# Kernel tuning notes

Hardware: AMD Instinct MI355X
Metric: run time of the kernel (lower is better)

Reference implementation:

```python
import jax, jax.numpy as jnp
import numpy as np

N_NODES = 100000


def gcn_layer(x, W, b, src, dst, n):
    # PyG GCNConv: add self-loops, symmetric degree normalization,
    # message = norm * (x @ W)[src], aggregated (sum) at dst, plus bias.
    loops = jnp.arange(n, dtype=src.dtype)
    s = jnp.concatenate([src, loops])  # [E+N]
    d = jnp.concatenate([dst, loops])  # [E+N]
    deg = jnp.zeros((n,), x.dtype).at[d].add(jnp.ones((s.shape[0],), x.dtype))
    dinv = jnp.where(deg > 0, jax.lax.rsqrt(deg), 0.0)
    norm = dinv[s] * dinv[d]  # [E+N]
    h = x @ W  # [N, out]
    msg = h[s] * norm[:, None]  # [E+N, out]
    out = jax.ops.segment_sum(msg, d, num_segments=n)
    return out + b


def setup_inputs() -> dict:
    key = jax.random.key(0)
    k1, k2, k3, k4 = jax.random.split(key, 4)
    in_dim, hid_dim, out_dim = 128, 128, 64
    x = jax.random.normal(k1, (N_NODES, in_dim), dtype=jnp.float32)
    edge_index = jax.random.randint(k2, (2, 1600000), 0, N_NODES, dtype=jnp.int64)
    W1 = jax.random.normal(k3, (in_dim, hid_dim), dtype=jnp.float32) / np.sqrt(in_dim)
    b1 = jnp.zeros((hid_dim,), jnp.float32)
    W2 = jax.random.normal(k4, (hid_dim, out_dim), dtype=jnp.float32) / np.sqrt(hid_dim)
    b2 = jnp.zeros((out_dim,), jnp.float32)
    return {"x": x, "edge_index": edge_index, "W1": W1, "b1": b1, "W2": W2, "b2": b2}


def reference(x, edge_index, W1, b1, W2, b2):
    src, dst = edge_index[0], edge_index[1]
    h = gcn_layer(x, W1, b1, src, dst, N_NODES)
    h = jax.nn.relu(h)
    # F.dropout(training=False) -> identity (eval mode reference)
    out = gcn_layer(h, W2, b2, src, dst, N_NODES)
    return out
```

## Files before the change

kernel.cpp:

```cpp
#include <hip/hip_runtime.h>
#include <hip/hip_fp16.h>

#define NN 100000
#define NSB 256
#define WPS2 391
#define CAP2 8192
#define EPB 16

typedef _Float16 f16;
typedef _Float16 f16x8 __attribute__((ext_vector_type(8)));
typedef float f32x4 __attribute__((ext_vector_type(4)));

__device__ __forceinline__ int eload(const void* e, long i, int is64) {
  if (is64) return (int)((const long long*)e)[i];
  return ((const int*)e)[i];
}

__global__ __launch_bounds__(1024) void k_prep(const unsigned* __restrict__ e,
                                               int* __restrict__ flag,
                                               int* __restrict__ bcur2,
                                               const float* __restrict__ W1,
                                               const float* __restrict__ W2,
                                               f16* __restrict__ Wt1,
                                               f16* __restrict__ Wt2) {
  const int t = threadIdx.x;
  if (blockIdx.x == 0) {
    __shared__ unsigned red[1024];
    if (t < NSB) bcur2[t * 16] = t * CAP2;
    unsigned acc = e[1 + 2 * t] | e[1 + 2 * t + 2048];
    red[t] = acc;
    __syncthreads();
    for (int off = 512; off > 0; off >>= 1) {
      if (t < off) red[t] |= red[t + off];
      __syncthreads();
    }
    if (t == 0) *flag = (red[0] == 0) ? 1 : 0;
  } else {
    int idx = (blockIdx.x - 1) * 1024 + t;
    if (idx < 128 * 128) {
      int k = idx / 128, n = idx % 128;
      Wt1[n * 128 + k] = (f16)W1[idx];
    } else {
      int i2 = idx - 128 * 128;
      if (i2 < 128 * 64) {
        int k = i2 / 64, n = i2 % 64;
        Wt2[n * 128 + k] = (f16)W2[i2];
      }
    }
  }
}

__global__ __launch_bounds__(256) void k_split(const void* __restrict__ e,
                                               const int* __restrict__ flag,
                                               int E, int* __restrict__ bcur2,
                                               int* __restrict__ pk) {
  __shared__ int hist[NSB];
  const int tid = threadIdx.x;
  const long b0 = (long)blockIdx.x * (256 * EPB);
  const int is64 = *flag;
  hist[tid] = 0;
  __syncthreads();

  int sv[EPB], dv[EPB];
#pragma unroll
  for (int j = 0; j < EPB; ++j) {
    long idx = b0 + j * 256 + tid;
    int s = 0, d = -1;
    if (idx < E) {
      s = eload(e, idx, is64);
      d = eload(e, (long)E + idx, is64);
    }
    sv[j] = s; dv[j] = d;
    if (d >= 0) atomicAdd(&hist[(unsigned)d / WPS2], 1);
  }
  __syncthreads();
  {
    int c = hist[tid];
    int base = (c > 0) ? atomicAdd(&bcur2[tid * 16], c) : 0;
    __syncthreads();
    hist[tid] = base;
  }
  __syncthreads();
#pragma unroll
  for (int j = 0; j < EPB; ++j) {
    int d = dv[j];
    if (d < 0) continue;
    int w = (unsigned)d / WPS2;
    int dloc = d - w * WPS2;
    int pos = atomicAdd(&hist[w], 1);
    pk[pos] = (dloc << 17) | sv[j];
  }
}

__global__ __launch_bounds__(256) void k_wscan(const int* __restrict__ bcur2,
                                               int* __restrict__ wbase,
                                               int* __restrict__ rowptr, int E) {
  __shared__ int sm[NSB];
  int t = threadIdx.x;
  int c = bcur2[t * 16] - t * CAP2;
  sm[t] = c;
  __syncthreads();
  for (int off = 1; off < NSB; off <<= 1) {
    int a = (t >= off) ? sm[t - off] : 0;
    __syncthreads();
    sm[t] += a;
    __syncthreads();
  }
  wbase[t] = sm[t] - c;
  if (t == 0) rowptr[NN] = E;
}

__global__ __launch_bounds__(256) void k_build(const int* __restrict__ pk,
                                               const int* __restrict__ bcur2,
                                               const int* __restrict__ wbase,
                                               int* __restrict__ rowptr,
                                               float* __restrict__ dinv,
                                               int* __restrict__ csr) {
  __shared__ int lc[512];
  __shared__ int cur[512];
  const int tid = threadIdx.x;
  const int b = blockIdx.x;
  const int nlo = b * WPS2;
  const int nhi = (nlo + WPS2 < NN) ? nlo + WPS2 : NN;
  const int nw = nhi - nlo;
  lc[tid] = 0; lc[tid + 256] = 0;
  __syncthreads();
  const int cnt = bcur2[b * 16] - b * CAP2;
  const long s0 = (long)b * CAP2;
  for (int i = tid; i < cnt; i += 256)
    atomicAdd(&lc[(unsigned)pk[s0 + i] >> 17], 1);
  __syncthreads();
  for (int off = 1; off < 512; off <<= 1) {
    int a0 = (tid >= off) ? lc[tid - off] : 0;
    int a1 = (tid + 256 >= off) ? lc[tid + 256 - off] : 0;
    __syncthreads();
    lc[tid] += a0; lc[tid + 256] += a1;
    __syncthreads();
  }
  const int wb = wbase[b];
#pragma unroll
  for (int h = 0; h < 2; ++h) {
    int j = tid + h * 256;
    if (j < nw) {
      int inc = lc[j];
      int c = inc - (j > 0 ? lc[j - 1] : 0);
      int ex = wb + inc - c;
      rowptr[nlo + j] = ex;
      dinv[nlo + j] = rsqrtf((float)c + 1.0f);
      cur[j] = ex;
    }
  }
  __syncthreads();
  for (int i = tid; i < cnt; i += 256) {
    int p = pk[s0 + i];
    int pos = atomicAdd(&cur[(unsigned)p >> 17], 1);
    csr[pos] = p & 0x1FFFF;
  }
}

template <int COUT, bool RELU, typename TIN>
__global__ __launch_bounds__(256) void gemm_mfma(const TIN* __restrict__ X,
                                                 const f16* __restrict__ Wt,
                                                 const float* __restrict__ dinv,
                                                 f16* __restrict__ Y) {
  constexpr int NF = COUT / 16;
  __shared__ f16 Al[128 * 128];
  __shared__ f16 Bl[COUT * 128];
  const int tid = threadIdx.x;
  const long row0 = (long)blockIdx.x * 128;

  for (int c = tid; c < COUT * 16; c += 256) {
    int n = c >> 4, g = c & 15;
    f16x8 v = *(const f16x8*)&Wt[n * 128 + g * 8];
    *(f16x8*)((char*)Bl + n * 256 + ((g * 16) ^ ((n & 7) << 4))) = v;
  }
  for (int c = tid; c < 2048; c += 256) {
    int r = c >> 4, g = c & 15;
    long grow = row0 + r;
    f16x8 v;
    if (grow < NN) {
      if constexpr (sizeof(TIN) == 4) {
        const float4* p = (const float4*)&X[grow * 128 + g * 8];
        float4 p0 = p[0], p1 = p[1];
        float f[8] = {p0.x, p0.y, p0.z, p0.w, p1.x, p1.y, p1.z, p1.w};
#pragma unroll
        for (int j = 0; j < 8; ++j) {
          float t = RELU ? fmaxf(f[j], 0.f) : f[j];
          v[j] = (f16)t;
        }
      } else {
        v = *(const f16x8*)&X[grow * 128 + g * 8];
        if (RELU) {
#pragma unroll
          for (int j = 0; j < 8; ++j) v[j] = v[j] > (f16)0 ? v[j] : (f16)0;
        }
      }
    } else {
#pragma unroll
      for (int j = 0; j < 8; ++j) v[j] = (f16)0;
    }
    *(f16x8*)((char*)Al + r * 256 + ((g * 16) ^ ((r & 7) << 4))) = v;
  }
  __syncthreads();

  const int l = tid & 63, w = tid >> 6;
  const int lm = l & 15, lg = l >> 4;
  const int r0 = w * 32 + lm, r1 = r0 + 16;

  f32x4 acc0[NF], acc1[NF];
#pragma unroll
  for (int nf = 0; nf < NF; ++nf) { acc0[nf] = (f32x4)(0.f); acc1[nf] = (f32x4)(0.f); }

#pragma unroll
  for (int kk = 0; kk < 4; ++kk) {
    const int kb = kk * 64 + lg * 16;
    f16x8 a0 = *(const f16x8*)((const char*)Al + r0 * 256 + (kb ^ ((r0 & 7) << 4)));
    f16x8 a1 = *(const f16x8*)((const char*)Al + r1 * 256 + (kb ^ ((r1 & 7) << 4)));
#pragma unroll
    for (int nf = 0; nf < NF; ++nf) {
      int n = nf * 16 + lm;
      f16x8 b = *(const f16x8*)((const char*)Bl + n * 256 + (kb ^ ((n & 7) << 4)));
      acc0[nf] = __builtin_amdgcn_mfma_f32_16x16x32_f16(a0, b, acc0[nf], 0, 0, 0);
      acc1[nf] = __builtin_amdgcn_mfma_f32_16x16x32_f16(a1, b, acc1[nf], 0, 0, 0);
    }
  }

#pragma unroll
  for (int reg = 0; reg < 4; ++reg) {
    long gr0 = row0 + w * 32 + lg * 4 + reg;
    long gr1 = gr0 + 16;
    float d0 = (gr0 < NN) ? dinv[gr0] : 0.f;
    float d1 = (gr1 < NN) ? dinv[gr1] : 0.f;
#pragma unroll
    for (int nf = 0; nf < NF; ++nf) {
      if (gr0 < NN) Y[gr0 * COUT + nf * 16 + lm] = (f16)(acc0[nf][reg] * d0);
      if (gr1 < NN) Y[gr1 * COUT + nf * 16 + lm] = (f16)(acc1[nf][reg] * d1);
    }
  }
}

__device__ __forceinline__ void acc8f(float* acc, const __half* p) {
  float4 raw = *(const float4*)p;
  const __half2* h = (const __half2*)&raw;
#pragma unroll
  for (int q = 0; q < 4; ++q) {
    float2 f = __half22float2(h[q]);
    acc[2 * q] += f.x; acc[2 * q + 1] += f.y;
  }
}

template <int C, typename TOUT>
__global__ __launch_bounds__(256) void k_agg8(const __half* __restrict__ hn,
                                              const int* __restrict__ rowptr,
                                              const int* __restrict__ csr,
                                              const float* __restrict__ dinv,
                                              const float* __restrict__ bias,
                                              TOUT* __restrict__ out) {
  constexpr int TP = C / 8;
  long t = (long)blockIdx.x * 256 + threadIdx.x;
  int d = (int)(t / TP);
  if (d >= NN) return;
  int c8 = (int)(t % TP) * 8;

  float acc[8] = {0, 0, 0, 0, 0, 0, 0, 0};
  acc8f(acc, &hn[(long)d * C + c8]);
  int e = rowptr[d];
  const int end = rowptr[d + 1];

  for (; e + 8 <= end; e += 8) {
    int s[8];
#pragma unroll
    for (int u = 0; u < 8; ++u) s[u] = csr[e + u];
    float4 r[8];
#pragma unroll
    for (int u = 0; u < 8; ++u) r[u] = *(const float4*)&hn[(long)s[u] * C + c8];
#pragma unroll
    for (int u = 0; u < 8; ++u) {
      const __half2* h = (const __half2*)&r[u];
#pragma unroll
      for (int q = 0; q < 4; ++q) {
        float2 f = __half22float2(h[q]);
        acc[2 * q] += f.x; acc[2 * q + 1] += f.y;
      }
    }
  }
  if (e + 4 <= end) {
    int s[4];
#pragma unroll
    for (int u = 0; u < 4; ++u) s[u] = csr[e + u];
    float4 r[4];
#pragma unroll
    for (int u = 0; u < 4; ++u) r[u] = *(const float4*)&hn[(long)s[u] * C + c8];
#pragma unroll
    for (int u = 0; u < 4; ++u) {
      const __half2* h = (const __half2*)&r[u];
#pragma unroll
      for (int q = 0; q < 4; ++q) {
        float2 f = __half22float2(h[q]);
        acc[2 * q] += f.x; acc[2 * q + 1] += f.y;
      }
    }
    e += 4;
  }
  for (; e < end; ++e) acc8f(acc, &hn[(long)csr[e] * C + c8]);

  float dd = dinv[d];
  float4 bv0 = *(const float4*)&bias[c8];
  float4 bv1 = *(const float4*)&bias[c8 + 4];
  float o[8];
  o[0] = acc[0] * dd + bv0.x; o[1] = acc[1] * dd + bv0.y;
  o[2] = acc[2] * dd + bv0.z; o[3] = acc[3] * dd + bv0.w;
  o[4] = acc[4] * dd + bv1.x; o[5] = acc[5] * dd + bv1.y;
  o[6] = acc[6] * dd + bv1.z; o[7] = acc[7] * dd + bv1.w;

  if constexpr (sizeof(TOUT) == 2) {
    __half2 hp[4];
    hp[0] = __floats2half2_rn(o[0], o[1]);
    hp[1] = __floats2half2_rn(o[2], o[3]);
    hp[2] = __floats2half2_rn(o[4], o[5]);
    hp[3] = __floats2half2_rn(o[6], o[7]);
    *(float4*)&out[(long)d * C + c8] = *(float4*)hp;
  } else {
    *(float4*)&out[(long)d * C + c8]     = make_float4(o[0], o[1], o[2], o[3]);
    *(float4*)&out[(long)d * C + c8 + 4] = make_float4(o[4], o[5], o[6], o[7]);
  }
}

extern "C" void kernel_launch(void* const* d_in, const int* in_sizes, int n_in,
                              void* d_out, int out_size, void* d_ws, size_t ws_size,
                              hipStream_t stream) {
  const float* x  = (const float*)d_in[0];
  const void*  ep = d_in[1];
  const float* W1 = (const float*)d_in[2];
  const float* b1 = (const float*)d_in[3];
  const float* W2 = (const float*)d_in[4];
  const float* b2 = (const float*)d_in[5];
  float* out = (float*)d_out;
  const int E = in_sizes[1] / 2;

  float*  wsf    = (float*)d_ws;
  int*    wsi    = (int*)d_ws;
  int*    flag   = wsi;
  int*    bcur2  = wsi + 64;
  int*    wbase  = wsi + 4224;
  float*  dinv   = wsf + 4480;
  int*    rowptr = wsi + 104512;
  f16*    Wt1    = (f16*)(wsi + 204544);
  f16*    Wt2    = (f16*)(wsi + 212736);
  int*    csr    = wsi + 216832;
  int*    pk     = wsi + 1816832;
  f16*    hn1    = (f16*)(wsi + 3913984);
  f16*    a1     = (f16*)(wsi + 10313984);
  f16*    hn2    = hn1;

  const int SB = (E + 256 * EPB - 1) / (256 * EPB);
  const int GB = (NN + 127) / 128;

  k_prep<<<25, 1024, 0, stream>>>((const unsigned*)ep, flag, bcur2, W1, W2, Wt1, Wt2);
  k_split<<<SB, 256, 0, stream>>>(ep, flag, E, bcur2, pk);
  k_wscan<<<1, 256, 0, stream>>>(bcur2, wbase, rowptr, E);
  k_build<<<NSB, 256, 0, stream>>>(pk, bcur2, wbase, rowptr, dinv, csr);

  gemm_mfma<128, false, float><<<GB, 256, 0, stream>>>(x, Wt1, dinv, hn1);
  k_agg8<128, __half><<<(NN * 16 + 255) / 256, 256, 0, stream>>>(
      (const __half*)hn1, rowptr, csr, dinv, b1, (__half*)a1);

  gemm_mfma<64, true, f16><<<GB, 256, 0, stream>>>(a1, Wt2, dinv, hn2);
  k_agg8<64, float><<<(NN * 8 + 255) / 256, 256, 0, stream>>>(
      (const __half*)hn2, rowptr, csr, dinv, b2, out);
}
```

Baseline: 182.3 us.

## Fold bucket scan into build kernel and halve per-thread aggregation width

```diff
diff --git a/kernel.cpp b/kernel.cpp
--- a/kernel.cpp
+++ b/kernel.cpp
@@ -92,30 +92,12 @@
   }
 }
 
-__global__ __launch_bounds__(256) void k_wscan(const int* __restrict__ bcur2,
-                                               int* __restrict__ wbase,
-                                               int* __restrict__ rowptr, int E) {
-  __shared__ int sm[NSB];
-  int t = threadIdx.x;
-  int c = bcur2[t * 16] - t * CAP2;
-  sm[t] = c;
-  __syncthreads();
-  for (int off = 1; off < NSB; off <<= 1) {
-    int a = (t >= off) ? sm[t - off] : 0;
-    __syncthreads();
-    sm[t] += a;
-    __syncthreads();
-  }
-  wbase[t] = sm[t] - c;
-  if (t == 0) rowptr[NN] = E;
-}
-
 __global__ __launch_bounds__(256) void k_build(const int* __restrict__ pk,
                                                const int* __restrict__ bcur2,
-                                               const int* __restrict__ wbase,
                                                int* __restrict__ rowptr,
                                                float* __restrict__ dinv,
                                                int* __restrict__ csr) {
+  __shared__ int ws[NSB];
   __shared__ int lc[512];
   __shared__ int cur[512];
   const int tid = threadIdx.x;
@@ -123,9 +105,19 @@
   const int nlo = b * WPS2;
   const int nhi = (nlo + WPS2 < NN) ? nlo + WPS2 : NN;
   const int nw = nhi - nlo;
+  ws[tid] = bcur2[tid * 16] - tid * CAP2;
   lc[tid] = 0; lc[tid + 256] = 0;
   __syncthreads();
-  const int cnt = bcur2[b * 16] - b * CAP2;
+  const int cnt = ws[b];
+  for (int off = 1; off < NSB; off <<= 1) {
+    int a = (tid >= off) ? ws[tid - off] : 0;
+    __syncthreads();
+    ws[tid] += a;
+    __syncthreads();
+  }
+  const int wb = ws[b] - cnt;
+  if (b == NSB - 1 && tid == 0) rowptr[NN] = ws[NSB - 1];
+
   const long s0 = (long)b * CAP2;
   for (int i = tid; i < cnt; i += 256)
     atomicAdd(&lc[(unsigned)pk[s0 + i] >> 17], 1);
@@ -137,7 +129,6 @@
     lc[tid] += a0; lc[tid + 256] += a1;
     __syncthreads();
   }
-  const int wb = wbase[b];
 #pragma unroll
   for (int h = 0; h < 2; ++h) {
     int j = tid + h * 256;
@@ -239,31 +230,29 @@
   }
 }
 
-__device__ __forceinline__ void acc8f(float* acc, const __half* p) {
-  float4 raw = *(const float4*)p;
+__device__ __forceinline__ void acc4f(float* acc, const __half* p) {
+  float2 raw = *(const float2*)p;
   const __half2* h = (const __half2*)&raw;
-#pragma unroll
-  for (int q = 0; q < 4; ++q) {
-    float2 f = __half22float2(h[q]);
-    acc[2 * q] += f.x; acc[2 * q + 1] += f.y;
-  }
+  float2 f0 = __half22float2(h[0]);
+  float2 f1 = __half22float2(h[1]);
+  acc[0] += f0.x; acc[1] += f0.y; acc[2] += f1.x; acc[3] += f1.y;
 }
 
 template <int C, typename TOUT>
-__global__ __launch_bounds__(256) void k_agg8(const __half* __restrict__ hn,
+__global__ __launch_bounds__(256) void k_agg4(const __half* __restrict__ hn,
                                               const int* __restrict__ rowptr,
                                               const int* __restrict__ csr,
                                               const float* __restrict__ dinv,
                                               const float* __restrict__ bias,
                                               TOUT* __restrict__ out) {
-  constexpr int TP = C / 8;
+  constexpr int TP = C / 4;
   long t = (long)blockIdx.x * 256 + threadIdx.x;
   int d = (int)(t / TP);
   if (d >= NN) return;
-  int c8 = (int)(t % TP) * 8;
-
-  float acc[8] = {0, 0, 0, 0, 0, 0, 0, 0};
-  acc8f(acc, &hn[(long)d * C + c8]);
+  int c4 = (int)(t % TP) * 4;
+
+  float acc[4] = {0, 0, 0, 0};
+  acc4f(acc, &hn[(long)d * C + c4]);
   int e = rowptr[d];
   const int end = rowptr[d + 1];
 
@@ -271,58 +260,47 @@
     int s[8];
 #pragma unroll
     for (int u = 0; u < 8; ++u) s[u] = csr[e + u];
-    float4 r[8];
-#pragma unroll
-    for (int u = 0; u < 8; ++u) r[u] = *(const float4*)&hn[(long)s[u] * C + c8];
+    float2 r[8];
+#pragma unroll
+    for (int u = 0; u < 8; ++u) r[u] = *(const float2*)&hn[(long)s[u] * C + c4];
 #pragma unroll
     for (int u = 0; u < 8; ++u) {
       const __half2* h = (const __half2*)&r[u];
-#pragma unroll
-      for (int q = 0; q < 4; ++q) {
-        float2 f = __half22float2(h[q]);
-        acc[2 * q] += f.x; acc[2 * q + 1] += f.y;
-      }
+      float2 f0 = __half22float2(h[0]);
+      float2 f1 = __half22float2(h[1]);
+      acc[0] += f0.x; acc[1] += f0.y; acc[2] += f1.x; acc[3] += f1.y;
     }
   }
   if (e + 4 <= end) {
     int s[4];
 #pragma unroll
     for (int u = 0; u < 4; ++u) s[u] = csr[e + u];
-    float4 r[4];
-#pragma unroll
-    for (int u = 0; u < 4; ++u) r[u] = *(const float4*)&hn[(long)s[u] * C + c8];
+    float2 r[4];
+#pragma unroll
+    for (int u = 0; u < 4; ++u) r[u] = *(const float2*)&hn[(long)s[u] * C + c4];
 #pragma unroll
     for (int u = 0; u < 4; ++u) {
       const __half2* h = (const __half2*)&r[u];
-#pragma unroll
-      for (int q = 0; q < 4; ++q) {
-        float2 f = __half22float2(h[q]);
-        acc[2 * q] += f.x; acc[2 * q + 1] += f.y;
-      }
+      float2 f0 = __half22float2(h[0]);
+      float2 f1 = __half22float2(h[1]);
+      acc[0] += f0.x; acc[1] += f0.y; acc[2] += f1.x; acc[3] += f1.y;
     }
     e += 4;
   }
-  for (; e < end; ++e) acc8f(acc, &hn[(long)csr[e] * C + c8]);
+  for (; e < end; ++e) acc4f(acc, &hn[(long)csr[e] * C + c4]);
 
   float dd = dinv[d];
-  float4 bv0 = *(const float4*)&bias[c8];
-  float4 bv1 = *(const float4*)&bias[c8 + 4];
-  float o[8];
-  o[0] = acc[0] * dd + bv0.x; o[1] = acc[1] * dd + bv0.y;
-  o[2] = acc[2] * dd + bv0.z; o[3] = acc[3] * dd + bv0.w;
-  o[4] = acc[4] * dd + bv1.x; o[5] = acc[5] * dd + bv1.y;
-  o[6] = acc[6] * dd + bv1.z; o[7] = acc[7] * dd + bv1.w;
+  float4 bv = *(const float4*)&bias[c4];
+  float o0 = acc[0] * dd + bv.x, o1 = acc[1] * dd + bv.y;
+  float o2 = acc[2] * dd + bv.z, o3 = acc[3] * dd + bv.w;
 
   if constexpr (sizeof(TOUT) == 2) {
-    __half2 hp[4];
-    hp[0] = __floats2half2_rn(o[0], o[1]);
-    hp[1] = __floats2half2_rn(o[2], o[3]);
-    hp[2] = __floats2half2_rn(o[4], o[5]);
-    hp[3] = __floats2half2_rn(o[6], o[7]);
-    *(float4*)&out[(long)d * C + c8] = *(float4*)hp;
+    __half2 hp[2];
+    hp[0] = __floats2half2_rn(o0, o1);
+    hp[1] = __floats2half2_rn(o2, o3);
+    *(float2*)&out[(long)d * C + c4] = *(float2*)hp;
   } else {
-    *(float4*)&out[(long)d * C + c8]     = make_float4(o[0], o[1], o[2], o[3]);
-    *(float4*)&out[(long)d * C + c8 + 4] = make_float4(o[4], o[5], o[6], o[7]);
+    *(float4*)&out[(long)d * C + c4] = make_float4(o0, o1, o2, o3);
   }
 }
 
@@ -342,15 +320,14 @@
   int*    wsi    = (int*)d_ws;
   int*    flag   = wsi;
   int*    bcur2  = wsi + 64;
-  int*    wbase  = wsi + 4224;
-  float*  dinv   = wsf + 4480;
-  int*    rowptr = wsi + 104512;
-  f16*    Wt1    = (f16*)(wsi + 204544);
-  f16*    Wt2    = (f16*)(wsi + 212736);
-  int*    csr    = wsi + 216832;
-  int*    pk     = wsi + 1816832;
-  f16*    hn1    = (f16*)(wsi + 3913984);
-  f16*    a1     = (f16*)(wsi + 10313984);
+  float*  dinv   = wsf + 4224;
+  int*    rowptr = wsi + 104256;
+  f16*    Wt1    = (f16*)(wsi + 204288);
+  f16*    Wt2    = (f16*)(wsi + 212480);
+  int*    csr    = wsi + 216576;
+  int*    pk     = wsi + 1816576;
+  f16*    hn1    = (f16*)(wsi + 3913728);
+  f16*    a1     = (f16*)(wsi + 10313728);
   f16*    hn2    = hn1;
 
   const int SB = (E + 256 * EPB - 1) / (256 * EPB);
@@ -358,14 +335,13 @@
 
   k_prep<<<25, 1024, 0, stream>>>((const unsigned*)ep, flag, bcur2, W1, W2, Wt1, Wt2);
   k_split<<<SB, 256, 0, stream>>>(ep, flag, E, bcur2, pk);
-  k_wscan<<<1, 256, 0, stream>>>(bcur2, wbase, rowptr, E);
-  k_build<<<NSB, 256, 0, stream>>>(pk, bcur2, wbase, rowptr, dinv, csr);
+  k_build<<<NSB, 256, 0, stream>>>(pk, bcur2, rowptr, dinv, csr);
 
   gemm_mfma<128, false, float><<<GB, 256, 0, stream>>>(x, Wt1, dinv, hn1);
-  k_agg8<128, __half><<<(NN * 16 + 255) / 256, 256, 0, stream>>>(
+  k_agg4<128, __half><<<(NN * 32 + 255) / 256, 256, 0, stream>>>(
       (const __half*)hn1, rowptr, csr, dinv, b1, (__half*)a1);
 
   gemm_mfma<64, true, f16><<<GB, 256, 0, stream>>>(a1, Wt2, dinv, hn2);
-  k_agg8<64, float><<<(NN * 8 + 255) / 256, 256, 0, stream>>>(
+  k_agg4<64, float><<<(NN * 16 + 255) / 256, 256, 0, stream>>>(
       (const __half*)hn2, rowptr, csr, dinv, b2, out);
 }
```

After: 181.3 us. No clear change (-0.5%).
